# Optimization experiments

Measured on AMD Instinct MI355X. Metric: run time of the kernel, lower is better.

## Reference

```python
import jax, jax.numpy as jnp
import numpy as np

B = 16
D = 512
LENGTHS = [2048 + 256 * i for i in range(B)]  # sum = 63488 tokens (incl. cls per bag)


def _index_maps(lengths):
    # Static (numpy) index maps for ragged <-> padded layout. Each bag's row 0 is a
    # cls token (left untouched); rows 1..L-1 are the conv body.
    lengths = [int(l) for l in np.asarray(lengths).tolist()]
    offs = np.cumsum([0] + lengths)
    lens_b = [l - 1 for l in lengths]            # body lengths after removing cls
    Lmax = max(lens_b)
    Bn = len(lengths)
    pad_src = np.zeros((Bn, Lmax), dtype=np.int32)   # flat x row gathered into [b,t]
    pad_mask = np.zeros((Bn, Lmax), dtype=np.float32)
    body_pos_list, body_b_list, body_t_list = [], [], []
    for i, L in enumerate(lens_b):
        rows = np.arange(offs[i] + 1, offs[i] + 1 + L)
        pad_src[i, :L] = rows
        pad_mask[i, :L] = 1.0
        body_pos_list.append(rows)
        body_b_list.append(np.full(L, i, dtype=np.int32))
        body_t_list.append(np.arange(L, dtype=np.int32))
    body_pos = np.concatenate(body_pos_list)   # flat positions of body tokens
    body_b = np.concatenate(body_b_list)
    body_t = np.concatenate(body_t_list)
    return pad_src, pad_mask, body_pos, body_b, body_t


def _dwconv(xp, w, b):
    # Depthwise 'same' conv1d. xp: [B, D, Lmax], w: [D, 1, k] (torch layout), b: [D].
    y = jax.lax.conv_general_dilated(
        xp, w, window_strides=(1,), padding='SAME',
        feature_group_count=xp.shape[1],
        dimension_numbers=('NCH', 'OIH', 'NCH'))
    return y + b[None, :, None]


def setup_inputs():
    key = jax.random.key(0)
    ks = jax.random.split(key, 7)
    total = sum(LENGTHS)
    x = jax.random.normal(ks[0], (total, D), jnp.float32)
    def u(k, shape, fan):  # torch Conv1d default init: U(-1/sqrt(fan_in*k), ...)
        bound = 1.0 / np.sqrt(fan)
        return jax.random.uniform(k, shape, jnp.float32, -bound, bound)
    w3, b3 = u(ks[1], (D, 1, 3), 3), u(ks[2], (D,), 3)
    w5, b5 = u(ks[3], (D, 1, 5), 5), u(ks[4], (D,), 5)
    w7, b7 = u(ks[5], (D, 1, 7), 7), u(ks[6], (D,), 7)
    lengths = np.array(LENGTHS, dtype=np.int64)
    return {'x': x, 'w3': w3, 'b3': b3, 'w5': w5, 'b5': b5,
            'w7': w7, 'b7': b7, 'lengths': lengths}


def reference(x, w3, b3, w5, b5, w7, b7, lengths):
    pad_src, pad_mask, body_pos, body_b, body_t = _index_maps(lengths)
    # Gather ragged bodies into zero-padded [B, Lmax, D]; zero padding reproduces
    # the per-segment 'same' conv boundary behavior exactly.
    xb = x[pad_src] * pad_mask[:, :, None]
    xp = jnp.transpose(xb, (0, 2, 1))  # [B, D, Lmax]
    y = xp + _dwconv(xp, w3, b3) + _dwconv(xp, w5, b5) + _dwconv(xp, w7, b7)
    body = jnp.transpose(y, (0, 2, 1))[body_b, body_t]  # flat [sum(len-1), D]
    # cls rows keep original x values; body rows replaced by residual conv sum.
    return x.at[body_pos].set(body)
```

## Files before the change

kernel.cpp:

```cpp
#include <hip/hip_runtime.h>

#define DCH 512
#define RPB 16

__global__ __launch_bounds__(128) void ppeg_dwconv_kernel(
    const float* __restrict__ x,
    const float* __restrict__ w3, const float* __restrict__ b3,
    const float* __restrict__ w5, const float* __restrict__ b5,
    const float* __restrict__ w7, const float* __restrict__ b7,
    const int* __restrict__ lengths,
    float* __restrict__ out, int n_rows, int n_bags)
{
    __shared__ int soff[32];
    if (threadIdx.x == 0) {
        int acc = 0;
        for (int i = 0; i < n_bags; ++i) { soff[i] = acc; acc += lengths[i]; }
        soff[n_bags] = acc;
    }
    __syncthreads();

    const int tid = threadIdx.x;
    const int c0  = tid * 4;

    float W[7][4], bias[4];
    #pragma unroll
    for (int q = 0; q < 4; ++q) {
        const int d = c0 + q;
        const float a0 = w7[d*7+0], a1 = w7[d*7+1], a2 = w7[d*7+2], a3 = w7[d*7+3],
                    a4 = w7[d*7+4], a5 = w7[d*7+5], a6 = w7[d*7+6];
        const float f0 = w5[d*5+0], f1 = w5[d*5+1], f2 = w5[d*5+2], f3 = w5[d*5+3], f4 = w5[d*5+4];
        const float e0 = w3[d*3+0], e1 = w3[d*3+1], e2 = w3[d*3+2];
        W[0][q] = a0;
        W[1][q] = a1 + f0;
        W[2][q] = a2 + f1 + e0;
        W[3][q] = a3 + f2 + e1 + 1.0f;
        W[4][q] = a4 + f3 + e2;
        W[5][q] = a5 + f4;
        W[6][q] = a6;
        bias[q] = b3[d] + b5[d] + b7[d];
    }

    const int r0 = blockIdx.x * RPB;
    if (r0 >= n_rows) return;

    int b = 0;
    while (b + 1 < n_bags && soff[b + 1] <= r0) ++b;

    float4 win[7];
    #pragma unroll
    for (int j = 0; j < 6; ++j) {
        const int rr = r0 - 3 + j;
        win[j] = (rr >= 0 && rr < n_rows)
                   ? *(const float4*)(x + (size_t)rr * DCH + c0)
                   : make_float4(0.f, 0.f, 0.f, 0.f);
    }

    for (int i = 0; i < RPB; ++i) {
        const int r = r0 + i;
        if (r >= n_rows) break;

        const int rr = r + 3;
        win[6] = (rr < n_rows)
                   ? *(const float4*)(x + (size_t)rr * DCH + c0)
                   : make_float4(0.f, 0.f, 0.f, 0.f);

        while (b + 1 < n_bags && soff[b + 1] <= r) ++b;
        const int t = r - soff[b] - 1;

        float4 o;
        if (t < 0) {
            o = win[3];
        } else {
            const int Lb1 = soff[b + 1] - soff[b] - 1;
            float acc0 = bias[0], acc1 = bias[1], acc2 = bias[2], acc3 = bias[3];
            #pragma unroll
            for (int dt = -3; dt <= 3; ++dt) {
                const bool valid = (t + dt >= 0) && (t + dt < Lb1);
                const float m = valid ? 1.0f : 0.0f;
                const float4 v = win[dt + 3];
                acc0 += m * W[dt + 3][0] * v.x;
                acc1 += m * W[dt + 3][1] * v.y;
                acc2 += m * W[dt + 3][2] * v.z;
                acc3 += m * W[dt + 3][3] * v.w;
            }
            o = make_float4(acc0, acc1, acc2, acc3);
        }

        *(float4*)(out + (size_t)r * DCH + c0) = o;

        #pragma unroll
        for (int j = 0; j < 6; ++j) win[j] = win[j + 1];
    }
}

extern "C" void kernel_launch(void* const* d_in, const int* in_sizes, int n_in,
                              void* d_out, int out_size, void* d_ws, size_t ws_size,
                              hipStream_t stream) {
    const float* x       = (const float*)d_in[0];
    const float* w3      = (const float*)d_in[1];
    const float* b3      = (const float*)d_in[2];
    const float* w5      = (const float*)d_in[3];
    const float* b5      = (const float*)d_in[4];
    const float* w7      = (const float*)d_in[5];
    const float* b7      = (const float*)d_in[6];
    const int*   lengths = (const int*)d_in[7];

    const int n_bags = in_sizes[7];
    const int n_rows = in_sizes[0] / DCH;
    float* out = (float*)d_out;

    const int nblocks = (n_rows + RPB - 1) / RPB;
    ppeg_dwconv_kernel<<<nblocks, 128, 0, stream>>>(
        x, w3, b3, w5, b5, w7, b7, lengths, out, n_rows, n_bags);
}
```

Measured before the change: 248.6 us.

## Preload full row window, remap blocks across XCDs, use nontemporal stores

All 22 input rows for the block are loaded into registers up front, before the bag-offset prefix and weight setup, so the loads overlap that setup. Block IDs are remapped so contiguous row ranges land on the same XCD, which should improve L2 reuse of the halo rows. The bag lookup becomes a binary search followed by a two-bag select, interior rows take an unmasked FMA path, and outputs are written with nontemporal stores. The cost is much higher register use for the window, which could reduce occupancy.

```diff
diff --git a/kernel.cpp b/kernel.cpp
--- a/kernel.cpp
+++ b/kernel.cpp
@@ -2,6 +2,9 @@
 
 #define DCH 512
 #define RPB 16
+#define NW  (RPB + 6)
+
+typedef float f32x4 __attribute__((ext_vector_type(4)));
 
 __global__ __launch_bounds__(128) void ppeg_dwconv_kernel(
     const float* __restrict__ x,
@@ -9,87 +12,117 @@
     const float* __restrict__ w5, const float* __restrict__ b5,
     const float* __restrict__ w7, const float* __restrict__ b7,
     const int* __restrict__ lengths,
-    float* __restrict__ out, int n_rows, int n_bags)
+    float* __restrict__ out, int n_rows, int n_bags, int nblocks)
 {
-    __shared__ int soff[32];
-    if (threadIdx.x == 0) {
+    __shared__ int soff[40];
+
+    const int tid = threadIdx.x;
+    const int c0  = tid * 4;
+
+    int bid = blockIdx.x;
+    {
+        const int nx = 8;
+        const int q  = nblocks / nx, rm = nblocks % nx;
+        const int xcd = bid % nx, idx = bid / nx;
+        bid = (xcd < rm ? xcd * (q + 1) : rm * (q + 1) + (xcd - rm) * q) + idx;
+    }
+    const int r0 = bid * RPB;
+    if (r0 >= n_rows) return;
+
+    float4 win[NW];
+    if (r0 >= 3 && r0 + RPB + 2 < n_rows) {
+        const float* xp = x + (size_t)(r0 - 3) * DCH + c0;
+        #pragma unroll
+        for (int j = 0; j < NW; ++j)
+            win[j] = *(const float4*)(xp + (size_t)j * DCH);
+    } else {
+        #pragma unroll
+        for (int j = 0; j < NW; ++j) {
+            const int rr = r0 - 3 + j;
+            win[j] = (rr >= 0 && rr < n_rows)
+                       ? *(const float4*)(x + (size_t)rr * DCH + c0)
+                       : make_float4(0.f, 0.f, 0.f, 0.f);
+        }
+    }
+
+    if (tid == 0) {
         int acc = 0;
         for (int i = 0; i < n_bags; ++i) { soff[i] = acc; acc += lengths[i]; }
         soff[n_bags] = acc;
     }
-    __syncthreads();
-
-    const int tid = threadIdx.x;
-    const int c0  = tid * 4;
 
     float W[7][4], bias[4];
     #pragma unroll
-    for (int q = 0; q < 4; ++q) {
-        const int d = c0 + q;
+    for (int q2 = 0; q2 < 4; ++q2) {
+        const int d = c0 + q2;
         const float a0 = w7[d*7+0], a1 = w7[d*7+1], a2 = w7[d*7+2], a3 = w7[d*7+3],
                     a4 = w7[d*7+4], a5 = w7[d*7+5], a6 = w7[d*7+6];
         const float f0 = w5[d*5+0], f1 = w5[d*5+1], f2 = w5[d*5+2], f3 = w5[d*5+3], f4 = w5[d*5+4];
         const float e0 = w3[d*3+0], e1 = w3[d*3+1], e2 = w3[d*3+2];
-        W[0][q] = a0;
-        W[1][q] = a1 + f0;
-        W[2][q] = a2 + f1 + e0;
-        W[3][q] = a3 + f2 + e1 + 1.0f;
-        W[4][q] = a4 + f3 + e2;
-        W[5][q] = a5 + f4;
-        W[6][q] = a6;
-        bias[q] = b3[d] + b5[d] + b7[d];
+        W[0][q2] = a0;
+        W[1][q2] = a1 + f0;
+        W[2][q2] = a2 + f1 + e0;
+        W[3][q2] = a3 + f2 + e1 + 1.0f;
+        W[4][q2] = a4 + f3 + e2;
+        W[5][q2] = a5 + f4;
+        W[6][q2] = a6;
+        bias[q2] = b3[d] + b5[d] + b7[d];
     }
 
-    const int r0 = blockIdx.x * RPB;
-    if (r0 >= n_rows) return;
+    __syncthreads();
 
     int b = 0;
-    while (b + 1 < n_bags && soff[b + 1] <= r0) ++b;
+    #pragma unroll
+    for (int s = 16; s >= 1; s >>= 1)
+        if (b + s < n_bags && soff[b + s] <= r0) b += s;
 
-    float4 win[7];
+    const int e0b = soff[b];
+    const int e1b = soff[b + 1];
+    const int e2b = (b + 2 <= n_bags) ? soff[b + 2] : e1b;
+
     #pragma unroll
-    for (int j = 0; j < 6; ++j) {
-        const int rr = r0 - 3 + j;
-        win[j] = (rr >= 0 && rr < n_rows)
-                   ? *(const float4*)(x + (size_t)rr * DCH + c0)
-                   : make_float4(0.f, 0.f, 0.f, 0.f);
-    }
-
     for (int i = 0; i < RPB; ++i) {
         const int r = r0 + i;
-        if (r >= n_rows) break;
+        if (r < n_rows) {
+            const bool nb   = (r >= e1b);
+            const int  offb = nb ? e1b : e0b;
+            const int  endb = nb ? e2b : e1b;
+            const int  t    = r - offb - 1;
+            const int  Lb1  = endb - offb - 1;
 
-        const int rr = r + 3;
-        win[6] = (rr < n_rows)
-                   ? *(const float4*)(x + (size_t)rr * DCH + c0)
-                   : make_float4(0.f, 0.f, 0.f, 0.f);
+            float4 o;
+            if (t < 0) {
+                o = win[i + 3];
+            } else if (t >= 3 && t + 3 < Lb1) {
+                float a0 = bias[0], a1 = bias[1], a2 = bias[2], a3 = bias[3];
+                #pragma unroll
+                for (int dt = 0; dt < 7; ++dt) {
+                    const float4 v = win[i + dt];
+                    a0 = fmaf(W[dt][0], v.x, a0);
+                    a1 = fmaf(W[dt][1], v.y, a1);
+                    a2 = fmaf(W[dt][2], v.z, a2);
+                    a3 = fmaf(W[dt][3], v.w, a3);
+                }
+                o = make_float4(a0, a1, a2, a3);
+            } else {
+                float a0 = bias[0], a1 = bias[1], a2 = bias[2], a3 = bias[3];
+                #pragma unroll
+                for (int dt = 0; dt < 7; ++dt) {
+                    const int  tp    = t + dt - 3;
+                    const bool valid = (tp >= 0) && (tp < Lb1);
+                    const float mm   = valid ? 1.0f : 0.0f;
+                    const float4 v = win[i + dt];
+                    a0 = fmaf(mm * W[dt][0], v.x, a0);
+                    a1 = fmaf(mm * W[dt][1], v.y, a1);
+                    a2 = fmaf(mm * W[dt][2], v.z, a2);
+                    a3 = fmaf(mm * W[dt][3], v.w, a3);
+                }
+                o = make_float4(a0, a1, a2, a3);
+            }
 
-        while (b + 1 < n_bags && soff[b + 1] <= r) ++b;
-        const int t = r - soff[b] - 1;
-
-        float4 o;
-        if (t < 0) {
-            o = win[3];
-        } else {
-            const int Lb1 = soff[b + 1] - soff[b] - 1;
-            float acc0 = bias[0], acc1 = bias[1], acc2 = bias[2], acc3 = bias[3];
-            #pragma unroll
-            for (int dt = -3; dt <= 3; ++dt) {
-                const bool valid = (t + dt >= 0) && (t + dt < Lb1);
-                const float m = valid ? 1.0f : 0.0f;
-                const float4 v = win[dt + 3];
-                acc0 += m * W[dt + 3][0] * v.x;
-                acc1 += m * W[dt + 3][1] * v.y;
-                acc2 += m * W[dt + 3][2] * v.z;
-                acc3 += m * W[dt + 3][3] * v.w;
-            }
-            o = make_float4(acc0, acc1, acc2, acc3);
+            f32x4 ov = {o.x, o.y, o.z, o.w};
+            __builtin_nontemporal_store(ov, (f32x4*)(out + (size_t)r * DCH + c0));
         }
-
-        *(float4*)(out + (size_t)r * DCH + c0) = o;
-
-        #pragma unroll
-        for (int j = 0; j < 6; ++j) win[j] = win[j + 1];
     }
 }
 
@@ -111,5 +144,5 @@
 
     const int nblocks = (n_rows + RPB - 1) / RPB;
     ppeg_dwconv_kernel<<<nblocks, 128, 0, stream>>>(
-        x, w3, b3, w5, b5, w7, b7, lengths, out, n_rows, n_bags);
+        x, w3, b3, w5, b5, w7, b7, lengths, out, n_rows, n_bags, nblocks);
 }
```

After: 245.8 us. No clear change (-1.1%).
